# Kernel optimization log

Hardware: AMD Instinct MI355X
Metric: run time of the kernel (lower is better)

The kernel has to match this reference:

```python
import jax, jax.numpy as jnp
from jax import lax
import numpy as np

T = 65536   # seq_len (one long utterance)
C = 8       # n_cgs (contour generators in graph)
F = 10      # n_features + n_context
H = 64      # GRU hidden size
NIN = 4     # rnn_inputs=None -> x_module[:, 1:5]
NOUT = 1    # n_output


def setup_inputs() -> dict:
    key = jax.random.key(0)
    ks = jax.random.split(key, 9)
    x = jax.random.normal(ks[0], (T, F, C), jnp.float32)
    cg_masks = jnp.ones((T, C), jnp.int32)
    contour_starts = jax.random.randint(ks[1], (T, C), 0, 2, jnp.int32)
    # first timestep of each cg must start a contour (original loop only
    # produces output from the first start onward)
    contour_starts = contour_starts.at[0].set(1)
    s = 1.0 / np.sqrt(H)
    u = lambda k, shp: jax.random.uniform(k, shp, jnp.float32, -s, s)
    W_ih = u(ks[2], (C, 3 * H, NIN))
    W_hh = u(ks[3], (C, 3 * H, H))
    b_ih = u(ks[4], (C, 3 * H))
    b_hh = u(ks[5], (C, 3 * H))
    W_out = u(ks[6], (C, NOUT, H))
    b_out = u(ks[7], (C, NOUT))
    return {"x": x, "cg_masks": cg_masks, "contour_starts": contour_starts,
            "W_ih": W_ih, "W_hh": W_hh, "b_ih": b_ih, "b_hh": b_hh,
            "W_out": W_out, "b_out": b_out}


def reference(x, cg_masks, contour_starts, W_ih, W_hh, b_ih, b_hh, W_out, b_out):
    # x: (T, F, C); select rnn input features 1:5 for every contour generator
    x4 = x[:, 1:5, :]                                   # (T, 4, C)
    # precompute input-to-hidden gates for all cgs at once: (T, C, 3H)
    gx = jnp.einsum('tfc,cgf->tcg', x4, W_ih) + b_ih
    starts = contour_starts == 1                        # (T, C) bool

    def step(h, inp):
        gx_t, start_t = inp                             # (C, 3H), (C,)
        # ragged segment boundary -> reset hidden state (h_module = None)
        h = jnp.where(start_t[:, None], jnp.zeros_like(h), h)
        gh = jnp.einsum('cgh,ch->cg', W_hh, h) + b_hh   # (C, 3H)
        r = jax.nn.sigmoid(gx_t[:, :H] + gh[:, :H])
        z = jax.nn.sigmoid(gx_t[:, H:2 * H] + gh[:, H:2 * H])
        n = jnp.tanh(gx_t[:, 2 * H:] + r * gh[:, 2 * H:])
        h_new = (1.0 - z) * n + z * h
        return h_new, h_new

    h0 = jnp.zeros((C, H), x.dtype)
    _, hs = lax.scan(step, h0, (gx, starts))            # hs: (T, C, H)
    out = jnp.einsum('tch,coh->tco', hs, W_out) + b_out  # (T, C, NOUT)
    # scatter-add of each segment's y_rnn into y; with all-ones masks the
    # segments tile [0, T) so this is the masked sum over contour generators
    active = (cg_masks == 1).astype(out.dtype)[..., None]  # (T, C, 1)
    y = jnp.sum(out * active, axis=1)                   # (T, NOUT)
    return y
```

## Files before the change

### kernel.cpp

```cpp
#include <hip/hip_runtime.h>

#define T_LEN 65536
#define C_CH 8
#define CLEN 16
#define NB 16
#define WIN (CLEN * NB)
#define NBLK 2048
#define SCANW 6
#define MAXB 32

typedef short bf16x8 __attribute__((ext_vector_type(8)));
typedef float f32x4 __attribute__((ext_vector_type(4)));
typedef unsigned int uint;
typedef uint u32x4 __attribute__((ext_vector_type(4)));
typedef unsigned long long u64;

#define MFMA32 __builtin_amdgcn_mfma_f32_16x16x32_bf16

#define SC_RZ 1.4426950408889634f
#define SC_N  2.8853900817779268f

__device__ __forceinline__ uint f2bf(float f) {
    uint u = __float_as_uint(f);
    return (u + 0x7FFFu + ((u >> 16) & 1u)) >> 16;
}
__device__ __forceinline__ uint pk(float a, float b) {
    return f2bf(a) | (f2bf(b) << 16);
}
__device__ __forceinline__ uint cvtpk(float lo, float hi) {
    uint r;
    asm("v_cvt_pk_bf16_f32 %0, %1, %2" : "=v"(r) : "v"(lo), "v"(hi));
    return r;
}
__device__ __forceinline__ float expneg(float x) { return __builtin_amdgcn_exp2f(-x); }
__device__ __forceinline__ bf16x8 mk8(uint a, uint b, uint c, uint d) {
    union { uint u[4]; bf16x8 v; } x;
    x.u[0] = a; x.u[1] = b; x.u[2] = c; x.u[3] = d;
    return x.v;
}
__device__ __forceinline__ bf16x8 q2b(u32x4 q) {
    union { u32x4 q; bf16x8 b; } u; u.q = q; return u.b;
}
__device__ __forceinline__ float rcpf(float v) { return __builtin_amdgcn_rcpf(v); }

__global__ __launch_bounds__(64, 2) void gru_mfma(
    const float* __restrict__ x,
    const int*   __restrict__ cg,
    const int*   __restrict__ cs,
    const float* __restrict__ W_ih,
    const float* __restrict__ W_hh,
    const float* __restrict__ b_ih,
    const float* __restrict__ b_hh,
    const float* __restrict__ W_out,
    const float* __restrict__ b_out,
    float* __restrict__ y)
{
    __shared__ u64 stw[SCANW], acw[SCANW];
    __shared__ int sb[NB + 1];
    __shared__ float yw[NB][MAXB + 1];
    __shared__ uint2 bxl[MAXB][NB];

    const int lane = threadIdx.x;
    const int l15 = lane & 15, l4 = lane >> 4;
    const int slot = blockIdx.x & 7;
    const int c    = (blockIdx.x >> 3) & 7;
    const int whi  = blockIdx.x >> 6;
    const int w    = whi * 8 + slot;
    const int RB   = w * WIN;

    for (int rr = 0; rr < SCANW; ++rr) {
        int t = RB + rr * 64 + lane;
        int sv = 0, av = 0;
        if (t < T_LEN) { sv = cs[t * C_CH + c]; av = cg[t * C_CH + c]; }
        u64 m1 = __ballot(sv == 1);
        u64 m2 = __ballot(av == 1);
        if (lane == 0) { stw[rr] = m1; acw[rr] = m2; }
    }
    __syncthreads();

    if (lane <= NB) {
        int rel = lane * CLEN;
        int q = rel >> 6, r0 = rel & 63;
        u64 m = stw[q] >> r0;
        int pos = -1;
        if (m) pos = rel + __ffsll(m) - 1;
        else {
            for (int q2 = q + 1; q2 < SCANW; ++q2)
                if (stw[q2]) { pos = (q2 << 6) + __ffsll(stw[q2]) - 1; break; }
        }
        int Sa;
        if (pos >= 0) Sa = RB + pos;
        else {
            int t = RB + SCANW * 64;
            while (t < T_LEN && cs[t * C_CH + c] != 1) ++t;
            Sa = t;
        }
        sb[lane] = min(Sa, T_LEN);
    }
    __syncthreads();

    const int S = sb[l15];
    const int len = sb[l15 + 1] - S;
    int Lmax = len;
#pragma unroll
    for (int o = 1; o < 16; o <<= 1) Lmax = max(Lmax, __shfl_xor(Lmax, o));

    const float* Wc = W_hh + c * 192 * 64;
    u32x4 AhA[12][2];
#pragma unroll
    for (int tm = 0; tm < 12; ++tm) {
        const float sc = (tm < 8) ? SC_RZ : SC_N;
#pragma unroll
        for (int kt = 0; kt < 2; ++kt) {
            const float* p = Wc + (16 * tm + l15) * 64 + 32 * kt + 4 * l4;
            float4 a = *(const float4*)p;
            float4 b = *(const float4*)(p + 16);
            AhA[tm][kt] = (u32x4){ pk(a.x * sc, a.y * sc), pk(a.z * sc, a.w * sc),
                                   pk(b.x * sc, b.y * sc), pk(b.z * sc, b.w * sc) };
            asm volatile("" : "+a"(AhA[tm][kt]));
        }
    }
    u32x4 WoA[2];
#pragma unroll
    for (int kt = 0; kt < 2; ++kt) {
        uint d0 = 0, d1 = 0, d2 = 0, d3 = 0;
        if (l15 == 0) {
            const float* wp = W_out + c * 64 + 32 * kt + 4 * l4;
            d0 = pk(wp[0], wp[1]);  d1 = pk(wp[2], wp[3]);
            d2 = pk(wp[16], wp[17]); d3 = pk(wp[18], wp[19]);
        }
        WoA[kt] = (u32x4){ d0, d1, d2, d3 };
        asm volatile("" : "+a"(WoA[kt]));
    }

    uint Axd[12][2];
#pragma unroll
    for (int tm = 0; tm < 12; ++tm) {
        const float sc = (tm < 8) ? SC_RZ : SC_N;
        int row = 16 * tm + l15;
        uint d0 = 0, d1 = 0;
        if (l4 == 0) {
            float4 wi4 = *(const float4*)(W_ih + (c * 192 + row) * 4);
            d0 = pk(wi4.x * sc, wi4.y * sc);
            d1 = pk(wi4.z * sc, wi4.w * sc);
        } else if (l4 == 1) {
            float bias = (tm < 8) ? (b_ih[c * 192 + row] + b_hh[c * 192 + row]) * SC_RZ
                                  : b_ih[c * 192 + row] * SC_N;
            d0 = f2bf(bias);
        }
        Axd[tm][0] = d0; Axd[tm][1] = d1;
    }
    f32x4 bhn4[4];
#pragma unroll
    for (int tn = 0; tn < 4; ++tn) {
        float4 v = *(const float4*)(b_hh + c * 192 + 128 + 16 * tn + 4 * l4);
        bhn4[tn] = (f32x4){v.x * SC_N, v.y * SC_N, v.z * SC_N, v.w * SC_N};
    }
    const float bo = b_out[c];

    uint B0[4], B1[4];
#pragma unroll
    for (int i = 0; i < 4; ++i) { B0[i] = 0u; B1[i] = 0u; }
    const uint bx_c0 = (l4 == 1) ? 0x00003F80u : 0u;
    const f32x4 z4 = {0.f, 0.f, 0.f, 0.f};

    for (int s0 = 0; s0 < Lmax; s0 += MAXB) {
        const int Lb = min(MAXB, Lmax - s0);

        const int npair = Lb * NB;
        for (int p = lane; p < npair; p += 64) {
            int s = p >> 4;
            int t = min(sb[p & 15] + s0 + s, T_LEN - 1);
            const float* xp = x + (size_t)t * 80 + 8 + c;
            bxl[s][p & 15] = make_uint2(pk(xp[0], xp[8]), pk(xp[16], xp[24]));
        }
        int off = (S - RB) + s0;
        int q = off >> 6, r0 = off & 63;
        u64 w0s = (q < SCANW) ? stw[q] : 0ull;
        u64 w1s = (q + 1 < SCANW) ? stw[q + 1] : 0ull;
        u64 ms = (w0s >> r0) | (r0 ? (w1s << (64 - r0)) : 0ull);
        __syncthreads();

        uint2 bxn = bxl[0][l15];

        for (int s = 0; s < Lb; ++s) {
            const uint2 bxc = bxn;
            if (s + 1 < Lb) bxn = bxl[s + 1][l15];

            const bool rst = (ms >> s) & 1;
#pragma unroll
            for (int i = 0; i < 4; ++i) {
                B0[i] = rst ? 0u : B0[i];
                B1[i] = rst ? 0u : B1[i];
            }

            const bf16x8 Bx  = mk8((lane < 16) ? bxc.x : bx_c0,
                                   (lane < 16) ? bxc.y : 0u, 0u, 0u);
            const bf16x8 Bh0 = mk8(B0[0], B0[1], B0[2], B0[3]);
            const bf16x8 Bh1 = mk8(B1[0], B1[1], B1[2], B1[3]);

            uint nB[8];
#pragma unroll
            for (int tm = 0; tm < 4; ++tm) {
                const int tz = tm + 4, tn = tm + 8;
                f32x4 ar = MFMA32(mk8(Axd[tm][0], Axd[tm][1], 0u, 0u), Bx, z4, 0, 0, 0);
                ar = MFMA32(q2b(AhA[tm][0]), Bh0, ar, 0, 0, 0);
                ar = MFMA32(q2b(AhA[tm][1]), Bh1, ar, 0, 0, 0);
                f32x4 az = MFMA32(mk8(Axd[tz][0], Axd[tz][1], 0u, 0u), Bx, z4, 0, 0, 0);
                az = MFMA32(q2b(AhA[tz][0]), Bh0, az, 0, 0, 0);
                az = MFMA32(q2b(AhA[tz][1]), Bh1, az, 0, 0, 0);
                f32x4 gx = MFMA32(mk8(Axd[tn][0], Axd[tn][1], 0u, 0u), Bx, z4, 0, 0, 0);
                f32x4 gh = MFMA32(q2b(AhA[tn][0]), Bh0, bhn4[tm], 0, 0, 0);
                gh = MFMA32(q2b(AhA[tn][1]), Bh1, gh, 0, 0, 0);

                float hv[4];
#pragma unroll
                for (int i = 0; i < 4; ++i) {
                    float Dr = 1.f + expneg(ar[i]);
                    float Dz = 1.f + expneg(az[i]);
                    float rc = rcpf(Dr * Dz);
                    float rr = rc * Dz;
                    float zz = rc * Dr;
                    float np2 = fmaf(rr, gh[i], gx[i]);
                    float nn = fmaf(2.f, rcpf(1.f + expneg(np2)), -1.f);
                    const uint bd = (tm < 2) ? B0[2 * (tm & 1) + (i >> 1)]
                                             : B1[2 * (tm & 1) + (i >> 1)];
                    const float hold = __uint_as_float((i & 1) ? (bd & 0xFFFF0000u)
                                                               : (bd << 16));
                    float hh = fmaf(zz, hold - nn, nn);
                    hv[i] = hh;
                }
                nB[2 * tm]     = cvtpk(hv[0], hv[1]);
                nB[2 * tm + 1] = cvtpk(hv[2], hv[3]);
            }
            B0[0] = nB[0]; B0[1] = nB[1]; B0[2] = nB[2]; B0[3] = nB[3];
            B1[0] = nB[4]; B1[1] = nB[5]; B1[2] = nB[6]; B1[3] = nB[7];

            const bf16x8 Bh0n = mk8(B0[0], B0[1], B0[2], B0[3]);
            const bf16x8 Bh1n = mk8(B1[0], B1[1], B1[2], B1[3]);
            f32x4 y4 = MFMA32(q2b(WoA[0]), Bh0n, z4, 0, 0, 0);
            y4 = MFMA32(q2b(WoA[1]), Bh1n, y4, 0, 0, 0);
            if (lane < 16 && (s0 + s) < len) yw[lane][s] = y4[0];
        }
        __syncthreads();

        for (int b = 0; b < NB; ++b) {
            int Sb = sb[b];
            int lenb = sb[b + 1] - Sb;
            int sg = s0 + lane;
            if (lane < Lb && sg < lenb) {
                int offa = (Sb - RB) + sg;
                int qa = offa >> 6;
                bool act;
                if (qa < SCANW) act = (acw[qa] >> (offa & 63)) & 1;
                else            act = cg[(Sb + sg) * C_CH + c] == 1;
                if (act) atomicAdd(&y[Sb + sg], yw[b][lane] + bo);
            }
        }
        __syncthreads();
    }
}

extern "C" void kernel_launch(void* const* d_in, const int* in_sizes, int n_in,
                              void* d_out, int out_size, void* d_ws, size_t ws_size,
                              hipStream_t stream) {
    const float* x     = (const float*)d_in[0];
    const int*   cg    = (const int*)  d_in[1];
    const int*   cs    = (const int*)  d_in[2];
    const float* W_ih  = (const float*)d_in[3];
    const float* W_hh  = (const float*)d_in[4];
    const float* b_ih  = (const float*)d_in[5];
    const float* b_hh  = (const float*)d_in[6];
    const float* W_out = (const float*)d_in[7];
    const float* b_out = (const float*)d_in[8];
    float* y = (float*)d_out;

    hipMemsetAsync(y, 0, (size_t)out_size * sizeof(float), stream);
    gru_mfma<<<NBLK, 64, 0, stream>>>(x, cg, cs, W_ih, W_hh, b_ih, b_hh,
                                      W_out, b_out, y);
}
```

Measured before the change: 82.29 us.

## Rebalance per-lane segment boundaries greedily using start bitmaps

After the initial boundary search, the block recomputes the 15 interior segment boundaries so the chunks between contour starts are closer to equal length. It greedily picks the last start within a length cap, trying progressively larger caps until all chunks fit. This is meant to cut Lmax, the longest serial recurrence among the 16 parallel lanes, and so shorten the sequential step loop. The cost is extra bitmap scanning before the main loop plus an added __syncthreads inside a uniform branch.

```diff
diff --git a/kernel.cpp b/kernel.cpp
--- a/kernel.cpp
+++ b/kernel.cpp
@@ -42,6 +42,25 @@
     union { u32x4 q; bf16x8 b; } u; u.q = q; return u.b;
 }
 __device__ __forceinline__ float rcpf(float v) { return __builtin_amdgcn_rcpf(v); }
+
+__device__ __forceinline__ int prev_start_le(u64 w0, u64 w1, u64 w2, u64 w3,
+                                             u64 w4, u64 w5, int X) {
+    auto msk = [](u64 w, int base, int X) -> u64 {
+        if (X < base) return 0ull;
+        int r = X - base;
+        u64 m = (r >= 63) ? ~0ull : ((1ull << (r + 1)) - 1ull);
+        return w & m;
+    };
+    u64 m5 = msk(w5, 320, X), m4 = msk(w4, 256, X), m3 = msk(w3, 192, X);
+    u64 m2 = msk(w2, 128, X), m1 = msk(w1, 64, X),  m0 = msk(w0, 0, X);
+    if (m5) return 320 + 63 - __builtin_clzll(m5);
+    if (m4) return 256 + 63 - __builtin_clzll(m4);
+    if (m3) return 192 + 63 - __builtin_clzll(m3);
+    if (m2) return 128 + 63 - __builtin_clzll(m2);
+    if (m1) return  64 + 63 - __builtin_clzll(m1);
+    if (m0) return        63 - __builtin_clzll(m0);
+    return -1;
+}
 
 __global__ __launch_bounds__(64, 2) void gru_mfma(
     const float* __restrict__ x,
@@ -96,6 +115,43 @@
             Sa = t;
         }
         sb[lane] = min(Sa, T_LEN);
+    }
+    __syncthreads();
+
+    {
+        const int rel0  = sb[0]  - RB;
+        const int rel16 = sb[NB] - RB;
+        if (rel16 > rel0 && rel16 <= SCANW * 64 && rel0 < SCANW * 64) {
+            const u64 w0 = stw[0], w1 = stw[1], w2 = stw[2];
+            const u64 w3 = stw[3], w4 = stw[4], w5 = stw[5];
+            const int span = rel16 - rel0;
+            const int L0 = (span + 15) >> 4;
+            int myb = 0;
+            bool done = false;
+#pragma unroll
+            for (int a = 0; a < 4; ++a) {
+                const int L = L0 + ((a == 0) ? 1 : (a == 1) ? 3 : (a == 2) ? 6 : 10);
+                if (done) continue;
+                int prev = rel0, mybt = 0;
+                bool ok = true;
+                for (int k = 1; k <= 15; ++k) {
+                    int bk;
+                    if (prev >= rel16) bk = rel16;
+                    else {
+                        int cap = min(prev + L, rel16);
+                        int nb = prev_start_le(w0, w1, w2, w3, w4, w5, cap);
+                        if (nb <= prev) { ok = false; nb = prev; }
+                        bk = nb;
+                    }
+                    if (lane == k) mybt = bk;
+                    prev = bk;
+                }
+                ok = ok && (rel16 - prev <= L);
+                if (ok) { done = true; myb = mybt; }
+            }
+            __syncthreads();
+            if (done && lane >= 1 && lane <= 15) sb[lane] = RB + myb;
+        }
     }
     __syncthreads();
 
```

New measurement: 74.60 us (median of 2 runs). 9.4% less time.
